# Optimization experiments

Measured on AMD Instinct MI355X. Metric: run time of the kernel, lower is better.

The kernel has to match this reference:

```python
import jax, jax.numpy as jnp
import numpy as np

TOKENS = 8192
IN_F = 4096
OUT_F = 4096
QMAX = 127.0  # int8 symmetric quant range
EPS = 1e-8


def setup_inputs() -> dict:
    key = jax.random.key(0)
    k1, k2, k3, k4 = jax.random.split(key, 4)
    x = jax.random.normal(k1, (TOKENS, IN_F), dtype=jnp.float32)
    # Pre-quantized int8 weight [out_features, in_features]
    weight_q = jax.random.randint(k2, (OUT_F, IN_F), -127, 128, dtype=jnp.int8)
    # Per-output-channel weight scales (realistic small magnitudes)
    weight_scale = jax.random.uniform(k3, (OUT_F,), dtype=jnp.float32) * 0.01 + 1e-3
    bias = jax.random.normal(k4, (OUT_F,), dtype=jnp.float32)
    return {"x": x, "weight_q": weight_q, "weight_scale": weight_scale, "bias": bias}


def reference(x, weight_q, weight_scale, bias):
    # Dynamic per-token symmetric int8 activation quantization
    absmax = jnp.max(jnp.abs(x), axis=-1, keepdims=True)           # [T, 1]
    x_scale = jnp.maximum(absmax, EPS) / QMAX                      # [T, 1]
    x_q = jnp.clip(jnp.round(x / x_scale), -QMAX, QMAX).astype(jnp.int8)
    acc = jax.lax.dot_general(
        x_q, weight_q,
        dimension_numbers=(((1,), (1,)), ((), ())),
        preferred_element_type=jnp.int32,
    )
    # Inline dequant: per-token activation scale * per-channel weight scale
    out = acc.astype(jnp.float32) * x_scale * weight_scale[None, :]
    out = out + bias[None, :]
    return out
```

## Files before the change

### kernel.cpp

```cpp
#include <hip/hip_runtime.h>
#include <cstdint>
#include <cstddef>

#define TOKENS 8192
#define IN_F   4096
#define OUT_F  4096
#define QMAXF  127.0f
#define EPSF   1e-8f

typedef int i32x4 __attribute__((ext_vector_type(4)));

#define NIT   32
#define SLOTB 32768
#define LDS_TOTAL (4 * SLOTB)

__device__ __forceinline__ void gload16(const void* g, void* l) {
    __builtin_amdgcn_global_load_lds(
        (const __attribute__((address_space(1))) void*)g,
        (__attribute__((address_space(3))) void*)l,
        16, 0, 0);
}

__device__ __forceinline__ void bar() {
    asm volatile("" ::: "memory");
    __builtin_amdgcn_s_barrier();
    asm volatile("" ::: "memory");
}

__device__ __forceinline__ void lgkm0_fence() {
    asm volatile("s_waitcnt lgkmcnt(0)" ::: "memory");
    __builtin_amdgcn_sched_barrier(0);
}

__device__ __forceinline__ int quant1(float v, float inv) {
    int q = (int)rintf(v * inv);
    q = q > 127 ? 127 : q;
    q = q < -127 ? -127 : q;
    return q;
}

__device__ __forceinline__ unsigned int pack4i(int a, int b, int c, int d) {
    return (unsigned int)(a & 255) | ((unsigned int)(b & 255) << 8) |
           ((unsigned int)(c & 255) << 16) | ((unsigned int)(d & 255) << 24);
}

__global__ __launch_bounds__(256) void quant_x_kernel(const float* __restrict__ x,
                                                      signed char* __restrict__ xq,
                                                      float* __restrict__ xscale) {
    const int t   = blockIdx.x;
    const int tid = threadIdx.x;
    const float* xr = x + (size_t)t * IN_F + tid * 16;

    float4 v[4];
    float am = 0.0f;
#pragma unroll
    for (int i = 0; i < 4; ++i) {
        v[i] = ((const float4*)xr)[i];
        am = fmaxf(am, fmaxf(fmaxf(fabsf(v[i].x), fabsf(v[i].y)),
                             fmaxf(fabsf(v[i].z), fabsf(v[i].w))));
    }
#pragma unroll
    for (int off = 32; off >= 1; off >>= 1)
        am = fmaxf(am, __shfl_xor(am, off));

    __shared__ float wmax[4];
    const int wid = tid >> 6, lane = tid & 63;
    if (lane == 0) wmax[wid] = am;
    __syncthreads();
    am = fmaxf(fmaxf(wmax[0], wmax[1]), fmaxf(wmax[2], wmax[3]));

    const float s   = fmaxf(am, EPSF) / QMAXF;
    const float inv = QMAXF / fmaxf(am, EPSF);
    if (tid == 0) xscale[t] = s;

    unsigned int w[4];
#pragma unroll
    for (int i = 0; i < 4; ++i) {
        w[i] = pack4i(quant1(v[i].x, inv), quant1(v[i].y, inv),
                      quant1(v[i].z, inv), quant1(v[i].w, inv));
    }
    *(uint4*)(xq + (size_t)t * IN_F + tid * 16) = make_uint4(w[0], w[1], w[2], w[3]);
}

__global__ __launch_bounds__(256) void pack_w_kernel(const int* __restrict__ w,
                                                     signed char* __restrict__ wq) {
    const size_t idx = (size_t)blockIdx.x * 256 + threadIdx.x;
    const int4* src = (const int4*)w + idx * 4;
    unsigned int o[4];
#pragma unroll
    for (int i = 0; i < 4; ++i) {
        int4 u = src[i];
        o[i] = pack4i(u.x, u.y, u.z, u.w);
    }
    ((uint4*)wq)[idx] = make_uint4(o[0], o[1], o[2], o[3]);
}

__global__ __launch_bounds__(512, 2) void gemm_kernel(const signed char* __restrict__ xq,
                                                      const signed char* __restrict__ wq,
                                                      const float* __restrict__ xscale,
                                                      const float* __restrict__ wscale,
                                                      const float* __restrict__ bias,
                                                      float* __restrict__ out) {
    extern __shared__ __align__(16) char lds[];

    const int tid  = threadIdx.x;
    const int wid  = tid >> 6;
    const int lane = tid & 63;
    const int wr   = wid >> 2;
    const int wc   = wid & 3;

    const int bid = blockIdx.x;
    const int swz = (bid & 7) * 64 + (bid >> 3);
    const int bm0 = (swz >> 4) * 256;
    const int bn0 = (swz & 15) * 256;

    const int srow = ((tid >> 6) << 4) + (tid & 15);
    const int sgrn = ((tid >> 4) & 3) << 4;
    const signed char* pA = xq + (size_t)(bm0 + srow) * IN_F + sgrn;
    const signed char* pB = wq + (size_t)(bn0 + srow) * IN_F + sgrn;
    const int ldst = tid * 16;

    const int lrd = (lane >> 4) * 256 + (lane & 15) * 16;
    int a_off[8], b_off[4];
#pragma unroll
    for (int mi = 0; mi < 8; ++mi) a_off[mi] = (wr * 8 + mi) * 1024 + lrd;
#pragma unroll
    for (int ni = 0; ni < 4; ++ni) b_off[ni] = 16384 + (wc * 4 + ni) * 1024 + lrd;

    i32x4 acc[8][4];
#pragma unroll
    for (int mi = 0; mi < 8; ++mi)
#pragma unroll
        for (int ni = 0; ni < 4; ++ni)
#pragma unroll
            for (int r = 0; r < 4; ++r) acc[mi][ni][r] = 0;

#pragma unroll
    for (int s = 0; s < 3; ++s) {
        char* S = lds + s * SLOTB;
        const int ko = s * 64;
        gload16(pA + ko,                         S + ldst);
        gload16(pA + (size_t)128 * IN_F + ko,    S + 8192 + ldst);
        gload16(pB + ko,                         S + 16384 + ldst);
        gload16(pB + (size_t)128 * IN_F + ko,    S + 24576 + ldst);
    }
    asm volatile("s_waitcnt vmcnt(8)" ::: "memory");
    bar();

    for (int t = 0; t < NIT; ++t) {
        const int h0 = 2 * t;
        const char* S0 = lds + (h0 & 3) * SLOTB;
        const char* S1 = lds + ((h0 + 1) & 3) * SLOTB;
        char* G0 = lds + ((h0 + 3) & 3) * SLOTB;
        char* G1 = lds + ((h0 + 4) & 3) * SLOTB;
        const bool st0 = (h0 + 3) < 64;
        const bool st1 = (h0 + 4) < 64;
        const int ko0 = (h0 + 3) * 64;
        const int ko1 = (h0 + 4) * 64;

        i32x4 a[4], b[4];

#pragma unroll
        for (int ni = 0; ni < 4; ++ni) b[ni] = *(const i32x4*)(S0 + b_off[ni]);
#pragma unroll
        for (int mi = 0; mi < 4; ++mi) a[mi] = *(const i32x4*)(S0 + a_off[mi]);
        if (st0) {
            gload16(pA + ko0,                      G0 + ldst);
            gload16(pA + (size_t)128 * IN_F + ko0, G0 + 8192 + ldst);
        }
        bar();
        lgkm0_fence();
        __builtin_amdgcn_s_setprio(1);
#pragma unroll
        for (int mi = 0; mi < 4; ++mi)
#pragma unroll
            for (int ni = 0; ni < 4; ++ni)
                acc[mi][ni] = __builtin_amdgcn_mfma_i32_16x16x64_i8(a[mi], b[ni], acc[mi][ni], 0, 0, 0);
        __builtin_amdgcn_s_setprio(0);
        bar();

#pragma unroll
        for (int mi = 0; mi < 4; ++mi) a[mi] = *(const i32x4*)(S0 + a_off[4 + mi]);
        if (st0) {
            gload16(pB + ko0,                      G0 + 16384 + ldst);
            gload16(pB + (size_t)128 * IN_F + ko0, G0 + 24576 + ldst);
        }
        bar();
        lgkm0_fence();
        __builtin_amdgcn_s_setprio(1);
#pragma unroll
        for (int mi = 0; mi < 4; ++mi)
#pragma unroll
            for (int ni = 0; ni < 4; ++ni)
                acc[4 + mi][ni] = __builtin_amdgcn_mfma_i32_16x16x64_i8(a[mi], b[ni], acc[4 + mi][ni], 0, 0, 0);
        __builtin_amdgcn_s_setprio(0);
        if (t < NIT - 1) {
            asm volatile("s_waitcnt vmcnt(8)" ::: "memory");
        } else {
            asm volatile("s_waitcnt vmcnt(0)" ::: "memory");
        }
        bar();

#pragma unroll
        for (int ni = 0; ni < 4; ++ni) b[ni] = *(const i32x4*)(S1 + b_off[ni]);
#pragma unroll
        for (int mi = 0; mi < 4; ++mi) a[mi] = *(const i32x4*)(S1 + a_off[mi]);
        if (st1) {
            gload16(pA + ko1,                      G1 + ldst);
            gload16(pA + (size_t)128 * IN_F + ko1, G1 + 8192 + ldst);
        }
        bar();
        lgkm0_fence();
        __builtin_amdgcn_s_setprio(1);
#pragma unroll
        for (int mi = 0; mi < 4; ++mi)
#pragma unroll
            for (int ni = 0; ni < 4; ++ni)
                acc[mi][ni] = __builtin_amdgcn_mfma_i32_16x16x64_i8(a[mi], b[ni], acc[mi][ni], 0, 0, 0);
        __builtin_amdgcn_s_setprio(0);
        bar();

#pragma unroll
        for (int mi = 0; mi < 4; ++mi) a[mi] = *(const i32x4*)(S1 + a_off[4 + mi]);
        if (st1) {
            gload16(pB + ko1,                      G1 + 16384 + ldst);
            gload16(pB + (size_t)128 * IN_F + ko1, G1 + 24576 + ldst);
        }
        bar();
        lgkm0_fence();
        __builtin_amdgcn_s_setprio(1);
#pragma unroll
        for (int mi = 0; mi < 4; ++mi)
#pragma unroll
            for (int ni = 0; ni < 4; ++ni)
                acc[4 + mi][ni] = __builtin_amdgcn_mfma_i32_16x16x64_i8(a[mi], b[ni], acc[4 + mi][ni], 0, 0, 0);
        __builtin_amdgcn_s_setprio(0);
        if (t < NIT - 2) {
            asm volatile("s_waitcnt vmcnt(8)" ::: "memory");
        } else if (t == NIT - 2) {
            asm volatile("s_waitcnt vmcnt(4)" ::: "memory");
        } else {
            asm volatile("s_waitcnt vmcnt(0)" ::: "memory");
        }
        bar();
    }

    const int l15 = lane & 15, lq = lane >> 4;
#pragma unroll
    for (int mi = 0; mi < 8; ++mi) {
        const int rbase = bm0 + wr * 128 + mi * 16 + lq * 4;
        float xsv[4];
#pragma unroll
        for (int j = 0; j < 4; ++j) xsv[j] = xscale[rbase + j];
#pragma unroll
        for (int ni = 0; ni < 4; ++ni) {
            const int col = bn0 + wc * 64 + ni * 16 + l15;
            const float wsc = wscale[col];
            const float bv  = bias[col];
#pragma unroll
            for (int j = 0; j < 4; ++j) {
                out[(size_t)(rbase + j) * OUT_F + col] =
                    (float)acc[mi][ni][j] * xsv[j] * wsc + bv;
            }
        }
    }
}

extern "C" void kernel_launch(void* const* d_in, const int* in_sizes, int n_in,
                              void* d_out, int out_size, void* d_ws, size_t ws_size,
                              hipStream_t stream) {
    const float* x      = (const float*)d_in[0];
    const int*   w      = (const int*)d_in[1];
    const float* wscale = (const float*)d_in[2];
    const float* bias   = (const float*)d_in[3];
    float* out = (float*)d_out;

    char* ws = (char*)d_ws;
    signed char* xq  = (signed char*)ws;
    signed char* wq8 = (signed char*)(ws + (size_t)TOKENS * IN_F);
    float* xscale    = (float*)(ws + (size_t)TOKENS * IN_F + (size_t)OUT_F * IN_F);

    hipFuncSetAttribute((const void*)gemm_kernel,
                        hipFuncAttributeMaxDynamicSharedMemorySize, LDS_TOTAL);

    quant_x_kernel<<<TOKENS, 256, 0, stream>>>(x, xq, xscale);
    pack_w_kernel<<<(OUT_F * (IN_F / 16)) / 256, 256, 0, stream>>>(w, wq8);
    gemm_kernel<<<(TOKENS / 256) * (OUT_F / 256), 512, LDS_TOTAL, stream>>>(
        xq, wq8, xscale, wscale, bias, out);
}
```

Baseline: 199.7 us.

## Software-pipeline LDS fragment reads behind MFMAs with scheduling group barriers

Restructures the GEMM main loop so the LDS fragment reads for the next half-step are issued while the current MFMA block runs. Register double-buffers the A and B fragments, halving barriers per half-step, and uses sched_group_barrier to interleave ds_reads with MFMAs. Out-of-range prefetches are clamped to the last k-chunk instead of being predicated off, which adds redundant loads but removes branches and allows uniform vmcnt waits. The cost is higher register pressure and a reliance on the interleave pattern being a good fit for the hardware.

```diff
diff --git a/kernel.cpp b/kernel.cpp
--- a/kernel.cpp
+++ b/kernel.cpp
@@ -30,6 +30,11 @@
 __device__ __forceinline__ void lgkm0_fence() {
     asm volatile("s_waitcnt lgkmcnt(0)" ::: "memory");
     __builtin_amdgcn_sched_barrier(0);
+}
+
+template <unsigned MASK, unsigned N>
+__device__ __forceinline__ void sgb() {
+    __builtin_amdgcn_sched_group_barrier(MASK, N, 0);
 }
 
 __device__ __forceinline__ int quant1(float v, float inv) {
@@ -139,111 +144,113 @@
     for (int s = 0; s < 3; ++s) {
         char* S = lds + s * SLOTB;
         const int ko = s * 64;
-        gload16(pA + ko,                         S + ldst);
-        gload16(pA + (size_t)128 * IN_F + ko,    S + 8192 + ldst);
-        gload16(pB + ko,                         S + 16384 + ldst);
-        gload16(pB + (size_t)128 * IN_F + ko,    S + 24576 + ldst);
+        gload16(pA + ko,                      S + ldst);
+        gload16(pA + (size_t)128 * IN_F + ko, S + 8192 + ldst);
+        gload16(pB + ko,                      S + 16384 + ldst);
+        gload16(pB + (size_t)128 * IN_F + ko, S + 24576 + ldst);
     }
     asm volatile("s_waitcnt vmcnt(8)" ::: "memory");
     bar();
 
+    i32x4 aC[4], aN[4], bA[4], bN[4];
+#pragma unroll
+    for (int ni = 0; ni < 4; ++ni) bA[ni] = *(const i32x4*)(lds + b_off[ni]);
+#pragma unroll
+    for (int mi = 0; mi < 4; ++mi) aC[mi] = *(const i32x4*)(lds + a_off[mi]);
+
     for (int t = 0; t < NIT; ++t) {
-        const int h0 = 2 * t;
-        const char* S0 = lds + (h0 & 3) * SLOTB;
-        const char* S1 = lds + ((h0 + 1) & 3) * SLOTB;
-        char* G0 = lds + ((h0 + 3) & 3) * SLOTB;
-        char* G1 = lds + ((h0 + 4) & 3) * SLOTB;
-        const bool st0 = (h0 + 3) < 64;
-        const bool st1 = (h0 + 4) < 64;
-        const int ko0 = (h0 + 3) * 64;
-        const int ko1 = (h0 + 4) * 64;
-
-        i32x4 a[4], b[4];
-
-#pragma unroll
-        for (int ni = 0; ni < 4; ++ni) b[ni] = *(const i32x4*)(S0 + b_off[ni]);
-#pragma unroll
-        for (int mi = 0; mi < 4; ++mi) a[mi] = *(const i32x4*)(S0 + a_off[mi]);
-        if (st0) {
-            gload16(pA + ko0,                      G0 + ldst);
-            gload16(pA + (size_t)128 * IN_F + ko0, G0 + 8192 + ldst);
-        }
-        bar();
-        lgkm0_fence();
-        __builtin_amdgcn_s_setprio(1);
-#pragma unroll
-        for (int mi = 0; mi < 4; ++mi)
-#pragma unroll
-            for (int ni = 0; ni < 4; ++ni)
-                acc[mi][ni] = __builtin_amdgcn_mfma_i32_16x16x64_i8(a[mi], b[ni], acc[mi][ni], 0, 0, 0);
-        __builtin_amdgcn_s_setprio(0);
-        bar();
-
-#pragma unroll
-        for (int mi = 0; mi < 4; ++mi) a[mi] = *(const i32x4*)(S0 + a_off[4 + mi]);
-        if (st0) {
-            gload16(pB + ko0,                      G0 + 16384 + ldst);
-            gload16(pB + (size_t)128 * IN_F + ko0, G0 + 24576 + ldst);
-        }
-        bar();
-        lgkm0_fence();
-        __builtin_amdgcn_s_setprio(1);
-#pragma unroll
-        for (int mi = 0; mi < 4; ++mi)
-#pragma unroll
-            for (int ni = 0; ni < 4; ++ni)
-                acc[4 + mi][ni] = __builtin_amdgcn_mfma_i32_16x16x64_i8(a[mi], b[ni], acc[4 + mi][ni], 0, 0, 0);
-        __builtin_amdgcn_s_setprio(0);
-        if (t < NIT - 1) {
-            asm volatile("s_waitcnt vmcnt(8)" ::: "memory");
-        } else {
-            asm volatile("s_waitcnt vmcnt(0)" ::: "memory");
-        }
-        bar();
-
-#pragma unroll
-        for (int ni = 0; ni < 4; ++ni) b[ni] = *(const i32x4*)(S1 + b_off[ni]);
-#pragma unroll
-        for (int mi = 0; mi < 4; ++mi) a[mi] = *(const i32x4*)(S1 + a_off[mi]);
-        if (st1) {
-            gload16(pA + ko1,                      G1 + ldst);
-            gload16(pA + (size_t)128 * IN_F + ko1, G1 + 8192 + ldst);
-        }
-        bar();
-        lgkm0_fence();
-        __builtin_amdgcn_s_setprio(1);
-#pragma unroll
-        for (int mi = 0; mi < 4; ++mi)
-#pragma unroll
-            for (int ni = 0; ni < 4; ++ni)
-                acc[mi][ni] = __builtin_amdgcn_mfma_i32_16x16x64_i8(a[mi], b[ni], acc[mi][ni], 0, 0, 0);
-        __builtin_amdgcn_s_setprio(0);
-        bar();
-
-#pragma unroll
-        for (int mi = 0; mi < 4; ++mi) a[mi] = *(const i32x4*)(S1 + a_off[4 + mi]);
-        if (st1) {
-            gload16(pB + ko1,                      G1 + 16384 + ldst);
-            gload16(pB + (size_t)128 * IN_F + ko1, G1 + 24576 + ldst);
-        }
-        bar();
-        lgkm0_fence();
-        __builtin_amdgcn_s_setprio(1);
-#pragma unroll
-        for (int mi = 0; mi < 4; ++mi)
-#pragma unroll
-            for (int ni = 0; ni < 4; ++ni)
-                acc[4 + mi][ni] = __builtin_amdgcn_mfma_i32_16x16x64_i8(a[mi], b[ni], acc[4 + mi][ni], 0, 0, 0);
-        __builtin_amdgcn_s_setprio(0);
-        if (t < NIT - 2) {
-            asm volatile("s_waitcnt vmcnt(8)" ::: "memory");
-        } else if (t == NIT - 2) {
-            asm volatile("s_waitcnt vmcnt(4)" ::: "memory");
-        } else {
-            asm volatile("s_waitcnt vmcnt(0)" ::: "memory");
-        }
-        bar();
-    }
+        const int h = 2 * t;
+        const char* S0 = lds + (h & 3) * SLOTB;
+        const char* S1 = lds + ((h + 1) & 3) * SLOTB;
+        const char* S2 = lds + ((h + 2) & 3) * SLOTB;
+        char* G3 = lds + ((h + 3) & 3) * SLOTB;
+        char* G4 = lds + ((h + 4) & 3) * SLOTB;
+        const int ko3 = (h + 3 < 64 ? h + 3 : 63) * 64;
+        const int ko4 = (h + 4 < 64 ? h + 4 : 63) * 64;
+
+        lgkm0_fence();
+        __builtin_amdgcn_s_setprio(1);
+        gload16(pA + ko3,                      G3 + ldst);
+        gload16(pA + (size_t)128 * IN_F + ko3, G3 + 8192 + ldst);
+#pragma unroll
+        for (int mi = 0; mi < 4; ++mi)
+#pragma unroll
+            for (int ni = 0; ni < 4; ++ni)
+                acc[mi][ni] = __builtin_amdgcn_mfma_i32_16x16x64_i8(aC[mi], bA[ni], acc[mi][ni], 0, 0, 0);
+#pragma unroll
+        for (int mi = 0; mi < 4; ++mi) aN[mi] = *(const i32x4*)(S0 + a_off[4 + mi]);
+        sgb<0x30, 2>();
+#pragma unroll
+        for (int g = 0; g < 4; ++g) { sgb<0x8, 2>(); sgb<0x100, 1>(); }
+        sgb<0x8, 8>();
+        __builtin_amdgcn_s_setprio(0);
+        __builtin_amdgcn_sched_barrier(0);
+        asm volatile("s_waitcnt vmcnt(6)" ::: "memory");
+        bar();
+
+        lgkm0_fence();
+        __builtin_amdgcn_s_setprio(1);
+        gload16(pB + ko3,                      G3 + 16384 + ldst);
+        gload16(pB + (size_t)128 * IN_F + ko3, G3 + 24576 + ldst);
+#pragma unroll
+        for (int mi = 0; mi < 4; ++mi)
+#pragma unroll
+            for (int ni = 0; ni < 4; ++ni)
+                acc[4 + mi][ni] = __builtin_amdgcn_mfma_i32_16x16x64_i8(aN[mi], bA[ni], acc[4 + mi][ni], 0, 0, 0);
+#pragma unroll
+        for (int ni = 0; ni < 4; ++ni) bN[ni] = *(const i32x4*)(S1 + b_off[ni]);
+#pragma unroll
+        for (int mi = 0; mi < 4; ++mi) aC[mi] = *(const i32x4*)(S1 + a_off[mi]);
+        sgb<0x30, 2>();
+#pragma unroll
+        for (int g = 0; g < 8; ++g) { sgb<0x8, 1>(); sgb<0x100, 1>(); }
+        sgb<0x8, 8>();
+        __builtin_amdgcn_s_setprio(0);
+        __builtin_amdgcn_sched_barrier(0);
+        bar();
+
+        lgkm0_fence();
+        __builtin_amdgcn_s_setprio(1);
+        gload16(pA + ko4,                      G4 + ldst);
+        gload16(pA + (size_t)128 * IN_F + ko4, G4 + 8192 + ldst);
+#pragma unroll
+        for (int mi = 0; mi < 4; ++mi)
+#pragma unroll
+            for (int ni = 0; ni < 4; ++ni)
+                acc[mi][ni] = __builtin_amdgcn_mfma_i32_16x16x64_i8(aC[mi], bN[ni], acc[mi][ni], 0, 0, 0);
+#pragma unroll
+        for (int mi = 0; mi < 4; ++mi) aN[mi] = *(const i32x4*)(S1 + a_off[4 + mi]);
+        sgb<0x30, 2>();
+#pragma unroll
+        for (int g = 0; g < 4; ++g) { sgb<0x8, 2>(); sgb<0x100, 1>(); }
+        sgb<0x8, 8>();
+        __builtin_amdgcn_s_setprio(0);
+        __builtin_amdgcn_sched_barrier(0);
+        asm volatile("s_waitcnt vmcnt(6)" ::: "memory");
+        bar();
+
+        lgkm0_fence();
+        __builtin_amdgcn_s_setprio(1);
+        gload16(pB + ko4,                      G4 + 16384 + ldst);
+        gload16(pB + (size_t)128 * IN_F + ko4, G4 + 24576 + ldst);
+#pragma unroll
+        for (int mi = 0; mi < 4; ++mi)
+#pragma unroll
+            for (int ni = 0; ni < 4; ++ni)
+                acc[4 + mi][ni] = __builtin_amdgcn_mfma_i32_16x16x64_i8(aN[mi], bN[ni], acc[4 + mi][ni], 0, 0, 0);
+#pragma unroll
+        for (int ni = 0; ni < 4; ++ni) bA[ni] = *(const i32x4*)(S2 + b_off[ni]);
+#pragma unroll
+        for (int mi = 0; mi < 4; ++mi) aC[mi] = *(const i32x4*)(S2 + a_off[mi]);
+        sgb<0x30, 2>();
+#pragma unroll
+        for (int g = 0; g < 8; ++g) { sgb<0x8, 1>(); sgb<0x100, 1>(); }
+        sgb<0x8, 8>();
+        __builtin_amdgcn_s_setprio(0);
+        __builtin_amdgcn_sched_barrier(0);
+        bar();
+    }
+    asm volatile("s_waitcnt vmcnt(0)" ::: "memory");
 
     const int l15 = lane & 15, lq = lane >> 4;
 #pragma unroll
@@ -280,8 +287,8 @@
     signed char* wq8 = (signed char*)(ws + (size_t)TOKENS * IN_F);
     float* xscale    = (float*)(ws + (size_t)TOKENS * IN_F + (size_t)OUT_F * IN_F);
 
-    hipFuncSetAttribute((const void*)gemm_kernel,
-                        hipFuncAttributeMaxDynamicSharedMemorySize, LDS_TOTAL);
+    (void)hipFuncSetAttribute((const void*)gemm_kernel,
+                              hipFuncAttributeMaxDynamicSharedMemorySize, LDS_TOTAL);
 
     quant_x_kernel<<<TOKENS, 256, 0, stream>>>(x, xq, xscale);
     pack_w_kernel<<<(OUT_F * (IN_F / 16)) / 256, 256, 0, stream>>>(w, wq8);
```

After: 208.9 us. 1.05x slower.

## Load A fragments directly from global into registers, stage only B in LDS

Applied to the files above, without the earlier changes.

The A (activation) tile is no longer staged through LDS. Each wave loads its MFMA A fragments straight from global memory into registers, double-buffered across k-steps. Only B goes through a 4-slot LDS ring of 64 KB, half the previous footprint, with fewer barriers per step. This removes LDS traffic and bank pressure for A and should allow higher occupancy, but the A reads are now uncoalesced 16-byte loads per lane with no sharing between waves, so redundant global/L2 traffic rises and latency is hidden only one step ahead.

```diff
diff --git a/kernel.cpp b/kernel.cpp
--- a/kernel.cpp
+++ b/kernel.cpp
@@ -9,10 +9,6 @@
 #define EPSF   1e-8f
 
 typedef int i32x4 __attribute__((ext_vector_type(4)));
-
-#define NIT   32
-#define SLOTB 32768
-#define LDS_TOTAL (4 * SLOTB)
 
 __device__ __forceinline__ void gload16(const void* g, void* l) {
     __builtin_amdgcn_global_load_lds(
@@ -101,11 +97,11 @@
                                                       const float* __restrict__ wscale,
                                                       const float* __restrict__ bias,
                                                       float* __restrict__ out) {
-    extern __shared__ __align__(16) char lds[];
+    __shared__ __align__(16) char Blds[4 * 16384];
 
     const int tid  = threadIdx.x;
+    const int lane = tid & 63;
     const int wid  = tid >> 6;
-    const int lane = tid & 63;
     const int wr   = wid >> 2;
     const int wc   = wid & 3;
 
@@ -116,16 +112,19 @@
 
     const int srow = ((tid >> 6) << 4) + (tid & 15);
     const int sgrn = ((tid >> 4) & 3) << 4;
-    const signed char* pA = xq + (size_t)(bm0 + srow) * IN_F + sgrn;
     const signed char* pB = wq + (size_t)(bn0 + srow) * IN_F + sgrn;
     const int ldst = tid * 16;
 
+    const signed char* pAblk = xq + (size_t)bm0 * IN_F;
+    int vA[8];
+#pragma unroll
+    for (int mi = 0; mi < 8; ++mi)
+        vA[mi] = (wr * 128 + mi * 16 + (lane & 15)) * IN_F + (lane >> 4) * 16;
+
     const int lrd = (lane >> 4) * 256 + (lane & 15) * 16;
-    int a_off[8], b_off[4];
-#pragma unroll
-    for (int mi = 0; mi < 8; ++mi) a_off[mi] = (wr * 8 + mi) * 1024 + lrd;
-#pragma unroll
-    for (int ni = 0; ni < 4; ++ni) b_off[ni] = 16384 + (wc * 4 + ni) * 1024 + lrd;
+    int b_off[4];
+#pragma unroll
+    for (int ni = 0; ni < 4; ++ni) b_off[ni] = (wc * 4 + ni) * 1024 + lrd;
 
     i32x4 acc[8][4];
 #pragma unroll
@@ -135,114 +134,104 @@
 #pragma unroll
             for (int r = 0; r < 4; ++r) acc[mi][ni][r] = 0;
 
-#pragma unroll
-    for (int s = 0; s < 3; ++s) {
-        char* S = lds + s * SLOTB;
-        const int ko = s * 64;
-        gload16(pA + ko,                         S + ldst);
-        gload16(pA + (size_t)128 * IN_F + ko,    S + 8192 + ldst);
-        gload16(pB + ko,                         S + 16384 + ldst);
-        gload16(pB + (size_t)128 * IN_F + ko,    S + 24576 + ldst);
-    }
-    asm volatile("s_waitcnt vmcnt(8)" ::: "memory");
+    gload16(pB,                           Blds + ldst);
+    gload16(pB + (size_t)128 * IN_F,      Blds + 8192 + ldst);
+    gload16(pB + 64,                      Blds + 16384 + ldst);
+    gload16(pB + (size_t)128 * IN_F + 64, Blds + 16384 + 8192 + ldst);
+
+    i32x4 aC[8], aN[8], b[4];
+#pragma unroll
+    for (int mi = 0; mi < 8; ++mi)
+        aC[mi] = *(const i32x4*)(pAblk + vA[mi]);
+
+    asm volatile("s_waitcnt vmcnt(0)" ::: "memory");
     bar();
 
-    for (int t = 0; t < NIT; ++t) {
+    for (int t = 0; t < 31; ++t) {
         const int h0 = 2 * t;
-        const char* S0 = lds + (h0 & 3) * SLOTB;
-        const char* S1 = lds + ((h0 + 1) & 3) * SLOTB;
-        char* G0 = lds + ((h0 + 3) & 3) * SLOTB;
-        char* G1 = lds + ((h0 + 4) & 3) * SLOTB;
-        const bool st0 = (h0 + 3) < 64;
-        const bool st1 = (h0 + 4) < 64;
-        const int ko0 = (h0 + 3) * 64;
-        const int ko1 = (h0 + 4) * 64;
-
-        i32x4 a[4], b[4];
-
-#pragma unroll
-        for (int ni = 0; ni < 4; ++ni) b[ni] = *(const i32x4*)(S0 + b_off[ni]);
-#pragma unroll
-        for (int mi = 0; mi < 4; ++mi) a[mi] = *(const i32x4*)(S0 + a_off[mi]);
-        if (st0) {
-            gload16(pA + ko0,                      G0 + ldst);
-            gload16(pA + (size_t)128 * IN_F + ko0, G0 + 8192 + ldst);
+
+        {
+            const char* S = Blds + (h0 & 3) * 16384;
+            const signed char* pAh = pAblk + (h0 + 1) * 64;
+#pragma unroll
+            for (int mi = 0; mi < 8; ++mi) aN[mi] = *(const i32x4*)(pAh + vA[mi]);
+            {
+                char* D = Blds + ((h0 + 2) & 3) * 16384;
+                const int ko = (h0 + 2) * 64;
+                gload16(pB + ko,                      D + ldst);
+                gload16(pB + (size_t)128 * IN_F + ko, D + 8192 + ldst);
+            }
+#pragma unroll
+            for (int ni = 0; ni < 4; ++ni) b[ni] = *(const i32x4*)(S + b_off[ni]);
+            lgkm0_fence();
+            __builtin_amdgcn_s_setprio(1);
+#pragma unroll
+            for (int mi = 0; mi < 8; ++mi)
+#pragma unroll
+                for (int ni = 0; ni < 4; ++ni)
+                    acc[mi][ni] = __builtin_amdgcn_mfma_i32_16x16x64_i8(aC[mi], b[ni], acc[mi][ni], 0, 0, 0);
+            __builtin_amdgcn_s_setprio(0);
+            asm volatile("s_waitcnt vmcnt(2)" ::: "memory");
+            bar();
         }
-        bar();
+
+        {
+            const int h1 = h0 + 1;
+            const char* S = Blds + (h1 & 3) * 16384;
+            const signed char* pAh = pAblk + (h1 + 1) * 64;
+#pragma unroll
+            for (int mi = 0; mi < 8; ++mi) aC[mi] = *(const i32x4*)(pAh + vA[mi]);
+            {
+                char* D = Blds + ((h1 + 2) & 3) * 16384;
+                const int ko = (h1 + 2) * 64;
+                gload16(pB + ko,                      D + ldst);
+                gload16(pB + (size_t)128 * IN_F + ko, D + 8192 + ldst);
+            }
+#pragma unroll
+            for (int ni = 0; ni < 4; ++ni) b[ni] = *(const i32x4*)(S + b_off[ni]);
+            lgkm0_fence();
+            __builtin_amdgcn_s_setprio(1);
+#pragma unroll
+            for (int mi = 0; mi < 8; ++mi)
+#pragma unroll
+                for (int ni = 0; ni < 4; ++ni)
+                    acc[mi][ni] = __builtin_amdgcn_mfma_i32_16x16x64_i8(aN[mi], b[ni], acc[mi][ni], 0, 0, 0);
+            __builtin_amdgcn_s_setprio(0);
+            asm volatile("s_waitcnt vmcnt(2)" ::: "memory");
+            bar();
+        }
+    }
+
+    {
+        const char* S = Blds + (62 & 3) * 16384;
+        const signed char* pAh = pAblk + 63 * 64;
+#pragma unroll
+        for (int mi = 0; mi < 8; ++mi) aN[mi] = *(const i32x4*)(pAh + vA[mi]);
+#pragma unroll
+        for (int ni = 0; ni < 4; ++ni) b[ni] = *(const i32x4*)(S + b_off[ni]);
         lgkm0_fence();
         __builtin_amdgcn_s_setprio(1);
 #pragma unroll
-        for (int mi = 0; mi < 4; ++mi)
+        for (int mi = 0; mi < 8; ++mi)
 #pragma unroll
             for (int ni = 0; ni < 4; ++ni)
-                acc[mi][ni] = __builtin_amdgcn_mfma_i32_16x16x64_i8(a[mi], b[ni], acc[mi][ni], 0, 0, 0);
+                acc[mi][ni] = __builtin_amdgcn_mfma_i32_16x16x64_i8(aC[mi], b[ni], acc[mi][ni], 0, 0, 0);
         __builtin_amdgcn_s_setprio(0);
+        asm volatile("s_waitcnt vmcnt(0)" ::: "memory");
         bar();
-
-#pragma unroll
-        for (int mi = 0; mi < 4; ++mi) a[mi] = *(const i32x4*)(S0 + a_off[4 + mi]);
-        if (st0) {
-            gload16(pB + ko0,                      G0 + 16384 + ldst);
-            gload16(pB + (size_t)128 * IN_F + ko0, G0 + 24576 + ldst);
-        }
-        bar();
+    }
+    {
+        const char* S = Blds + (63 & 3) * 16384;
+#pragma unroll
+        for (int ni = 0; ni < 4; ++ni) b[ni] = *(const i32x4*)(S + b_off[ni]);
         lgkm0_fence();
         __builtin_amdgcn_s_setprio(1);
 #pragma unroll
-        for (int mi = 0; mi < 4; ++mi)
+        for (int mi = 0; mi < 8; ++mi)
 #pragma unroll
             for (int ni = 0; ni < 4; ++ni)
-                acc[4 + mi][ni] = __builtin_amdgcn_mfma_i32_16x16x64_i8(a[mi], b[ni], acc[4 + mi][ni], 0, 0, 0);
+                acc[mi][ni] = __builtin_amdgcn_mfma_i32_16x16x64_i8(aN[mi], b[ni], acc[mi][ni], 0, 0, 0);
         __builtin_amdgcn_s_setprio(0);
-        if (t < NIT - 1) {
-            asm volatile("s_waitcnt vmcnt(8)" ::: "memory");
-        } else {
-            asm volatile("s_waitcnt vmcnt(0)" ::: "memory");
-        }
-        bar();
-
-#pragma unroll
-        for (int ni = 0; ni < 4; ++ni) b[ni] = *(const i32x4*)(S1 + b_off[ni]);
-#pragma unroll
-        for (int mi = 0; mi < 4; ++mi) a[mi] = *(const i32x4*)(S1 + a_off[mi]);
-        if (st1) {
-            gload16(pA + ko1,                      G1 + ldst);
-            gload16(pA + (size_t)128 * IN_F + ko1, G1 + 8192 + ldst);
-        }
-        bar();
-        lgkm0_fence();
-        __builtin_amdgcn_s_setprio(1);
-#pragma unroll
-        for (int mi = 0; mi < 4; ++mi)
-#pragma unroll
-            for (int ni = 0; ni < 4; ++ni)
-                acc[mi][ni] = __builtin_amdgcn_mfma_i32_16x16x64_i8(a[mi], b[ni], acc[mi][ni], 0, 0, 0);
-        __builtin_amdgcn_s_setprio(0);
-        bar();
-
-#pragma unroll
-        for (int mi = 0; mi < 4; ++mi) a[mi] = *(const i32x4*)(S1 + a_off[4 + mi]);
-        if (st1) {
-            gload16(pB + ko1,                      G1 + 16384 + ldst);
-            gload16(pB + (size_t)128 * IN_F + ko1, G1 + 24576 + ldst);
-        }
-        bar();
-        lgkm0_fence();
-        __builtin_amdgcn_s_setprio(1);
-#pragma unroll
-        for (int mi = 0; mi < 4; ++mi)
-#pragma unroll
-            for (int ni = 0; ni < 4; ++ni)
-                acc[4 + mi][ni] = __builtin_amdgcn_mfma_i32_16x16x64_i8(a[mi], b[ni], acc[4 + mi][ni], 0, 0, 0);
-        __builtin_amdgcn_s_setprio(0);
-        if (t < NIT - 2) {
-            asm volatile("s_waitcnt vmcnt(8)" ::: "memory");
-        } else if (t == NIT - 2) {
-            asm volatile("s_waitcnt vmcnt(4)" ::: "memory");
-        } else {
-            asm volatile("s_waitcnt vmcnt(0)" ::: "memory");
-        }
-        bar();
     }
 
     const int l15 = lane & 15, lq = lane >> 4;
@@ -280,11 +269,8 @@
     signed char* wq8 = (signed char*)(ws + (size_t)TOKENS * IN_F);
     float* xscale    = (float*)(ws + (size_t)TOKENS * IN_F + (size_t)OUT_F * IN_F);
 
-    hipFuncSetAttribute((const void*)gemm_kernel,
-                        hipFuncAttributeMaxDynamicSharedMemorySize, LDS_TOTAL);
-
     quant_x_kernel<<<TOKENS, 256, 0, stream>>>(x, xq, xscale);
     pack_w_kernel<<<(OUT_F * (IN_F / 16)) / 256, 256, 0, stream>>>(w, wq8);
-    gemm_kernel<<<(TOKENS / 256) * (OUT_F / 256), 512, LDS_TOTAL, stream>>>(
+    gemm_kernel<<<(TOKENS / 256) * (OUT_F / 256), 512, 0, stream>>>(
         xq, wq8, xscale, wscale, bias, out);
 }
```

New measurement: 399.2 us. 2x slower.
